# Performance work log

Hardware: AMD Instinct MI355X
Metric: run time of the kernel (lower is better)

Reference implementation:

```python
import jax, jax.numpy as jnp
import numpy as np


def get_mgrid(slen):
    # replicates bliss get_mgrid: np.mgrid / offset, dstack((y, x)), scaled by (slen-1)/slen
    offset = (slen - 1) / 2.0
    c = (np.arange(slen, dtype=np.float32) - offset) / offset  # in [-1, 1]
    g = np.zeros((slen, slen, 2), dtype=np.float32)
    g[:, :, 0] = c[None, :]  # x-coordinate (varies along width, axis 1)
    g[:, :, 1] = c[:, None]  # y-coordinate (varies along height, axis 0)
    return jnp.asarray(g * (slen - 1) / slen)


def grid_sample_bilinear_zeros(img, grid):
    # img: [N, C, H, W]; grid: [N, Ho, Wo, 2] with (x, y) normalized coords.
    # F.grid_sample(mode='bilinear', padding_mode='zeros', align_corners=True)
    N, C, H, W = img.shape
    ix = (grid[..., 0] + 1.0) * 0.5 * (W - 1)  # [N, Ho, Wo]
    iy = (grid[..., 1] + 1.0) * 0.5 * (H - 1)
    ix0 = jnp.floor(ix)
    iy0 = jnp.floor(iy)
    wx1 = ix - ix0
    wy1 = iy - iy0
    wx0 = 1.0 - wx1
    wy0 = 1.0 - wy1

    def corner(iy_f, ix_f, w):
        valid = ((ix_f >= 0) & (ix_f <= W - 1) & (iy_f >= 0) & (iy_f <= H - 1)).astype(img.dtype)
        ixc = jnp.clip(ix_f, 0, W - 1).astype(jnp.int32)
        iyc = jnp.clip(iy_f, 0, H - 1).astype(jnp.int32)

        def gather_one(im, iy1, ix1, m):
            # im: [C, H, W]; iy1/ix1/m: [Ho, Wo] -> [C, Ho, Wo]
            return im[:, iy1, ix1] * m[None]

        vals = jax.vmap(gather_one)(img, iyc, ixc, valid)  # [N, C, Ho, Wo]
        return vals * w[:, None, :, :]

    return (
        corner(iy0, ix0, wy0 * wx0)
        + corner(iy0, ix0 + 1.0, wy0 * wx1)
        + corner(iy0 + 1.0, ix0, wy1 * wx0)
        + corner(iy0 + 1.0, ix0 + 1.0, wy1 * wx1)
    )


def setup_inputs() -> dict:
    key = jax.random.key(0)
    k1, k2 = jax.random.split(key)
    n_ptiles, max_src, n_bands = 1024, 4, 5
    tile_slen, ptile_slen = 4, 52
    locs = jax.random.uniform(k1, (n_ptiles, max_src, 2), dtype=jnp.float32)
    sources = jax.random.normal(k2, (n_ptiles, max_src, n_bands, ptile_slen, ptile_slen), dtype=jnp.float32)
    return {"locs": locs, "sources": sources, "tile_slen": tile_slen, "ptile_slen": ptile_slen}


def reference(locs, sources, tile_slen, ptile_slen):
    n_ptiles, max_src, n_bands, s, _ = sources.shape
    # location transform (from _render_one_source)
    padding = (ptile_slen - tile_slen) / 2.0
    l = locs * (tile_slen / ptile_slen) + padding / ptile_slen
    l = (l - 0.5) * 2.0
    l_sw = l[..., ::-1]  # index_select with swap=[1,0]: (y,x) -> (x,y)
    mgrid = get_mgrid(ptile_slen)  # [P, P, 2]
    # grid for all sources at once: [n_ptiles, max_src, P, P, 2]
    grid = mgrid[None, None] - l_sw[:, :, None, None, :]
    imgs = sources.reshape(n_ptiles * max_src, n_bands, s, s)
    grid = grid.reshape(n_ptiles * max_src, ptile_slen, ptile_slen, 2)
    sampled = grid_sample_bilinear_zeros(imgs, grid)
    # accumulate over sources (the python loop + ptile += in the original)
    return sampled.reshape(n_ptiles, max_src, n_bands, ptile_slen, ptile_slen).sum(axis=1)
```

## Files before the change

### kernel.cpp

```cpp
#include <hip/hip_runtime.h>

constexpr int NP = 1024;
constexpr int MS = 4;
constexpr int NB = 5;
constexpr int SL = 52;
constexpr int SS = SL * SL;
constexpr int NF4 = SS / 4;
constexpr int NTHR = 256;
constexpr int NJ = (SS + NTHR - 1) / NTHR;
constexpr int BUF = SS + 4;

__device__ __forceinline__ void gload_lds16(const float* g, float* l) {
    __builtin_amdgcn_global_load_lds(
        (const __attribute__((address_space(1))) void*)g,
        (__attribute__((address_space(3))) void*)l,
        16, 0, 0);
}

__global__ __launch_bounds__(NTHR) void tile_render_kernel(
    const float* __restrict__ locs,
    const float* __restrict__ sources,
    float* __restrict__ out)
{
    __shared__ __align__(16) float smem[4 + 2 * BUF];
    float* const buf0 = smem + 4;
    float* const buf1 = smem + 4 + BUF;

    const int blk = blockIdx.x;
    const int p = blk / NB;
    const int b = blk - p * NB;
    const int tid = threadIdx.x;

    const float A = 25.5f / 26.0f;
    float bx[MS], by[MS];
    #pragma unroll
    for (int s = 0; s < MS; ++s) {
        float loc0 = locs[(p * MS + s) * 2 + 0];
        float loc1 = locs[(p * MS + s) * 2 + 1];
        float l0 = (loc0 * (4.0f / 52.0f) + (24.0f / 52.0f) - 0.5f) * 2.0f;
        float l1 = (loc1 * (4.0f / 52.0f) + (24.0f / 52.0f) - 0.5f) * 2.0f;
        bx[s] = (1.0f - l1) * 25.5f - 25.5f * 25.5f / 26.0f;
        by[s] = (1.0f - l0) * 25.5f - 25.5f * 25.5f / 26.0f;
    }

    const float* srcbase = sources + (size_t)p * MS * NB * SS + (size_t)b * SS;

    auto stage = [&](float* dst, int s) {
        const float* g = srcbase + (size_t)s * (NB * SS);
        gload_lds16(g + 4 * tid,          dst + 4 * tid);
        gload_lds16(g + 4 * (tid + NTHR), dst + 4 * (tid + NTHR));
        if (tid < NF4 - 2 * NTHR)
            gload_lds16(g + 4 * (tid + 2 * NTHR), dst + 4 * (tid + 2 * NTHR));
    };

    float acc[NJ];
    #pragma unroll
    for (int j = 0; j < NJ; ++j) acc[j] = 0.0f;

    stage(buf0, 0);

    #pragma unroll
    for (int s = 0; s < MS; ++s) {
        float* const cur = (s & 1) ? buf1 : buf0;
        float* const nxt = (s & 1) ? buf0 : buf1;
        __syncthreads();
        if (s < MS - 1) stage(nxt, s + 1);

        const float bxs = bx[s], bys = by[s];
        #pragma unroll
        for (int j = 0; j < NJ; ++j) {
            int pix = tid + j * NTHR;
            if (j == NJ - 1 && pix >= SS) continue;
            int y = pix / SL;
            int x = pix - y * SL;
            float ix = fmaf((float)x, A, bxs);
            float iy = fmaf((float)y, A, bys);
            float ix0f = floorf(ix);
            float iy0f = floorf(iy);
            float wx1 = ix - ix0f;
            float wy1 = iy - iy0f;
            float wx0 = 1.0f - wx1;
            float wy0 = 1.0f - wy1;
            int ix0 = (int)ix0f;
            int iy0 = (int)iy0f;
            float wxa = ((unsigned)ix0       <= 51u) ? wx0 : 0.0f;
            float wxb = ((unsigned)(ix0 + 1) <= 51u) ? wx1 : 0.0f;
            float wya = ((unsigned)iy0       <= 51u) ? wy0 : 0.0f;
            float wyb = ((unsigned)(iy0 + 1) <= 51u) ? wy1 : 0.0f;
            int bxi = min(max(ix0, -1), SL - 1);
            int r0 = min(max(iy0, 0), SL - 1);
            int r1 = min(max(iy0 + 1, 0), SL - 1);
            const float* p0 = cur + r0 * SL + bxi;
            const float* p1 = cur + r1 * SL + bxi;
            float v00 = p0[0], v01 = p0[1];
            float v10 = p1[0], v11 = p1[1];
            float h0 = fmaf(v01, wxb, v00 * wxa);
            float h1 = fmaf(v11, wxb, v10 * wxa);
            acc[j] = fmaf(h0, wya, acc[j]);
            acc[j] = fmaf(h1, wyb, acc[j]);
        }
    }

    float* outp = out + ((size_t)p * NB + b) * SS;
    #pragma unroll
    for (int j = 0; j < NJ; ++j) {
        int pix = tid + j * NTHR;
        if (pix < SS) outp[pix] = acc[j];
    }
}

extern "C" void kernel_launch(void* const* d_in, const int* in_sizes, int n_in,
                              void* d_out, int out_size, void* d_ws, size_t ws_size,
                              hipStream_t stream) {
    const float* locs = (const float*)d_in[0];
    const float* sources = (const float*)d_in[1];
    float* out = (float*)d_out;
    dim3 grid(NP * NB);
    dim3 block(NTHR);
    hipLaunchKernelGGL(tile_render_kernel, grid, block, 0, stream,
                       locs, sources, out);
}
```

Measured before the change: 56.13 us.

## Use zero-padded LDS tiles to drop bounds checks in bilinear sampling

Each source is now staged into a zero-padded LDS buffer (row stride 60, with a margin of rows and columns), so out-of-range bilinear corners read zeros and all clamping and validity masks go away. Loads switch from direct global-to-LDS to register float4 loads that are written into LDS after the compute, so the next source's load overlaps the current source's math. Per-pixel coordinates are precomputed once and the interpolation uses a lerp form with fewer multiplies. In exchange it needs an LDS zeroing pass, register staging of the loads, and relies on the source offsets staying within the padded margin.

```diff
diff --git a/kernel.cpp b/kernel.cpp
--- a/kernel.cpp
+++ b/kernel.cpp
@@ -5,31 +5,30 @@
 constexpr int NB = 5;
 constexpr int SL = 52;
 constexpr int SS = SL * SL;
-constexpr int NF4 = SS / 4;
 constexpr int NTHR = 256;
-constexpr int NJ = (SS + NTHR - 1) / NTHR;
-constexpr int BUF = SS + 4;
-
-__device__ __forceinline__ void gload_lds16(const float* g, float* l) {
-    __builtin_amdgcn_global_load_lds(
-        (const __attribute__((address_space(1))) void*)g,
-        (__attribute__((address_space(3))) void*)l,
-        16, 0, 0);
-}
+constexpr int NJ = 11;
+constexpr int TAIL = SS - (NJ - 1) * NTHR;
+constexpr int PST = 60;
+constexpr int PROWS = 56;
+constexpr int PX = 4;
+constexpr int PY = 2;
+constexpr int BUFF = PROWS * PST;
+constexpr int NCH = SS / 4;
 
 __global__ __launch_bounds__(NTHR) void tile_render_kernel(
     const float* __restrict__ locs,
     const float* __restrict__ sources,
     float* __restrict__ out)
 {
-    __shared__ __align__(16) float smem[4 + 2 * BUF];
-    float* const buf0 = smem + 4;
-    float* const buf1 = smem + 4 + BUF;
+    __shared__ __align__(16) float smem[2 * BUFF];
 
     const int blk = blockIdx.x;
     const int p = blk / NB;
     const int b = blk - p * NB;
     const int tid = threadIdx.x;
+
+    for (int i = 4 * tid; i < 2 * BUFF; i += 4 * NTHR)
+        *reinterpret_cast<float4*>(smem + i) = make_float4(0.f, 0.f, 0.f, 0.f);
 
     const float A = 25.5f / 26.0f;
     float bx[MS], by[MS];
@@ -43,61 +42,82 @@
         by[s] = (1.0f - l0) * 25.5f - 25.5f * 25.5f / 26.0f;
     }
 
-    const float* srcbase = sources + (size_t)p * MS * NB * SS + (size_t)b * SS;
+    float fx[NJ], fy[NJ];
+    #pragma unroll
+    for (int j = 0; j < NJ; ++j) {
+        int pix = tid + j * NTHR;
+        if (pix >= SS) pix = 0;
+        int y = pix / SL;
+        fx[j] = (float)(pix - y * SL);
+        fy[j] = (float)y;
+    }
 
-    auto stage = [&](float* dst, int s) {
-        const float* g = srcbase + (size_t)s * (NB * SS);
-        gload_lds16(g + 4 * tid,          dst + 4 * tid);
-        gload_lds16(g + 4 * (tid + NTHR), dst + 4 * (tid + NTHR));
-        if (tid < NF4 - 2 * NTHR)
-            gload_lds16(g + 4 * (tid + 2 * NTHR), dst + 4 * (tid + 2 * NTHR));
+    int woff[3];
+    bool has2;
+    {
+        #pragma unroll
+        for (int u = 0; u < 3; ++u) {
+            int c = tid + u * NTHR;
+            int cc = (c < NCH) ? c : 0;
+            int r = cc / 13;
+            woff[u] = (r + PY) * PST + PX + (cc - r * 13) * 4;
+        }
+        has2 = (tid < NCH - 2 * NTHR);
+    }
+
+    const float* gsrc = sources + ((size_t)p * MS * NB + b) * SS;
+
+    float4 ra, rb, rc;
+    auto issue = [&](int s) {
+        const float* g = gsrc + (size_t)s * (NB * SS);
+        ra = *reinterpret_cast<const float4*>(g + 4 * tid);
+        rb = *reinterpret_cast<const float4*>(g + 4 * (tid + NTHR));
+        if (has2) rc = *reinterpret_cast<const float4*>(g + 4 * (tid + 2 * NTHR));
+    };
+    auto write_lds = [&](float* buf) {
+        *reinterpret_cast<float4*>(buf + woff[0]) = ra;
+        *reinterpret_cast<float4*>(buf + woff[1]) = rb;
+        if (has2) *reinterpret_cast<float4*>(buf + woff[2]) = rc;
     };
 
     float acc[NJ];
     #pragma unroll
     for (int j = 0; j < NJ; ++j) acc[j] = 0.0f;
 
-    stage(buf0, 0);
+    issue(0);
+    __syncthreads();
+    write_lds(smem);
+    __syncthreads();
+
+    const float* const adj0 = smem + PY * PST + PX;
 
     #pragma unroll
     for (int s = 0; s < MS; ++s) {
-        float* const cur = (s & 1) ? buf1 : buf0;
-        float* const nxt = (s & 1) ? buf0 : buf1;
-        __syncthreads();
-        if (s < MS - 1) stage(nxt, s + 1);
+        if (s < MS - 1) issue(s + 1);
 
+        const float* adj = adj0 + ((s & 1) ? BUFF : 0);
         const float bxs = bx[s], bys = by[s];
         #pragma unroll
         for (int j = 0; j < NJ; ++j) {
-            int pix = tid + j * NTHR;
-            if (j == NJ - 1 && pix >= SS) continue;
-            int y = pix / SL;
-            int x = pix - y * SL;
-            float ix = fmaf((float)x, A, bxs);
-            float iy = fmaf((float)y, A, bys);
-            float ix0f = floorf(ix);
-            float iy0f = floorf(iy);
-            float wx1 = ix - ix0f;
-            float wy1 = iy - iy0f;
-            float wx0 = 1.0f - wx1;
-            float wy0 = 1.0f - wy1;
-            int ix0 = (int)ix0f;
-            int iy0 = (int)iy0f;
-            float wxa = ((unsigned)ix0       <= 51u) ? wx0 : 0.0f;
-            float wxb = ((unsigned)(ix0 + 1) <= 51u) ? wx1 : 0.0f;
-            float wya = ((unsigned)iy0       <= 51u) ? wy0 : 0.0f;
-            float wyb = ((unsigned)(iy0 + 1) <= 51u) ? wy1 : 0.0f;
-            int bxi = min(max(ix0, -1), SL - 1);
-            int r0 = min(max(iy0, 0), SL - 1);
-            int r1 = min(max(iy0 + 1, 0), SL - 1);
-            const float* p0 = cur + r0 * SL + bxi;
-            const float* p1 = cur + r1 * SL + bxi;
-            float v00 = p0[0], v01 = p0[1];
-            float v10 = p1[0], v11 = p1[1];
-            float h0 = fmaf(v01, wxb, v00 * wxa);
-            float h1 = fmaf(v11, wxb, v10 * wxa);
-            acc[j] = fmaf(h0, wya, acc[j]);
-            acc[j] = fmaf(h1, wyb, acc[j]);
+            float ix = fmaf(fx[j], A, bxs);
+            float iy = fmaf(fy[j], A, bys);
+            float ixf = floorf(ix);
+            float iyf = floorf(iy);
+            float wx = ix - ixf;
+            float wy = iy - iyf;
+            int xi = (int)ixf;
+            int yi = (int)iyf;
+            const float* q = adj + yi * PST + xi;
+            float v00 = q[0], v01 = q[1];
+            float v10 = q[PST], v11 = q[PST + 1];
+            float h0 = fmaf(wx, v01 - v00, v00);
+            float h1 = fmaf(wx, v11 - v10, v10);
+            acc[j] += fmaf(wy, h1 - h0, h0);
+        }
+
+        if (s < MS - 1) {
+            write_lds(smem + (((s + 1) & 1) ? BUFF : 0));
+            __syncthreads();
         }
     }
 
@@ -105,7 +125,7 @@
     #pragma unroll
     for (int j = 0; j < NJ; ++j) {
         int pix = tid + j * NTHR;
-        if (pix < SS) outp[pix] = acc[j];
+        if (j < NJ - 1 || tid < TAIL) outp[pix] = acc[j];
     }
 }
 
```

After: 96.45 us. 1.72x slower.
